# Kernel tuning notes

Hardware: AMD Instinct MI355X
Metric: run time of the kernel (lower is better)

Reference implementation:

```python
import jax, jax.numpy as jnp
import numpy as np

N_COMPANY = 16384
N_SECTOR = 64
PER_SECTOR = N_COMPANY // N_SECTOR  # 256, companies grouped contiguously by sector
WIN = 32
D_IN = 16
H_GRU = 64
H_INTRA = 64
H_INTER = 64
D_OUT = 4
E_INNER = 524288  # avg degree 32 within sectors


def setup_inputs() -> dict:
    key = jax.random.key(0)
    ks = jax.random.split(key, 20)
    s = 0.05

    daily_data_batch = jax.random.normal(ks[0], (WIN, N_COMPANY, D_IN), jnp.float32)

    rng = np.random.default_rng(0)
    dst = rng.integers(0, N_COMPANY, E_INNER)
    src = (dst // PER_SECTOR) * PER_SECTOR + rng.integers(0, PER_SECTOR, E_INNER)  # same-sector neighbors
    inner_edge = jnp.asarray(np.stack([src, dst]), jnp.int32)

    a, b = np.meshgrid(np.arange(N_SECTOR), np.arange(N_SECTOR), indexing="ij")
    oe = np.stack([a.ravel(), b.ravel()])
    oe = oe[:, oe[0] != oe[1]]  # fully-connected sector graph w/o self loops (GAT adds them)
    outer_edge = jnp.asarray(oe, jnp.int32)

    sector_ids = jnp.asarray(np.arange(N_COMPANY) // PER_SECTOR, jnp.int32)

    inp = {
        "daily_data_batch": daily_data_batch,
        "inner_edge": inner_edge,
        "outer_edge": outer_edge,
        "sector_ids": sector_ids,
        # BatchNorm1d(input_dim*window_size)
        "bn_gamma": jnp.ones((D_IN * WIN,), jnp.float32),
        "bn_beta": jnp.zeros((D_IN * WIN,), jnp.float32),
        # Graph GRU (per-node learnable initial hidden state)
        "gru_Wih": s * jax.random.normal(ks[1], (D_IN, 3 * H_GRU), jnp.float32),
        "gru_Whh": s * jax.random.normal(ks[2], (H_GRU, 3 * H_GRU), jnp.float32),
        "gru_bih": jnp.zeros((3 * H_GRU,), jnp.float32),
        "gru_bhh": jnp.zeros((3 * H_GRU,), jnp.float32),
        "gru_h0": s * jax.random.normal(ks[3], (N_COMPANY, H_GRU), jnp.float32),
        # intra-sector GATConv
        "gat1_W": s * jax.random.normal(ks[4], (H_GRU, H_INTRA), jnp.float32),
        "gat1_asrc": s * jax.random.normal(ks[5], (H_INTRA,), jnp.float32),
        "gat1_adst": s * jax.random.normal(ks[6], (H_INTRA,), jnp.float32),
        "gat1_b": jnp.zeros((H_INTRA,), jnp.float32),
        # inter-sector GATConv
        "gat2_W": s * jax.random.normal(ks[7], (H_INTRA, H_INTER), jnp.float32),
        "gat2_asrc": s * jax.random.normal(ks[8], (H_INTER,), jnp.float32),
        "gat2_adst": s * jax.random.normal(ks[9], (H_INTER,), jnp.float32),
        "gat2_b": jnp.zeros((H_INTER,), jnp.float32),
        # fusion / logit heads
        "fusion_W": s * jax.random.normal(ks[10], (H_GRU + H_INTRA + H_INTER, H_GRU), jnp.float32),
        "fusion_b": jnp.zeros((H_GRU,), jnp.float32),
        "logit_W": s * jax.random.normal(ks[11], (H_GRU, D_OUT), jnp.float32),
        "logit_b": jnp.zeros((D_OUT,), jnp.float32),
    }
    return inp


def _gat(x, edge, W, a_src, a_dst, b):
    """PyG-style single-head GATConv with default add_self_loops=True."""
    N = x.shape[0]
    h = x @ W  # [N, F]
    loops = jnp.arange(N, dtype=edge.dtype)
    src = jnp.concatenate([edge[0], loops])
    dst = jnp.concatenate([edge[1], loops])
    e = jax.nn.leaky_relu(h[src] @ a_src + h[dst] @ a_dst, 0.2)  # [E]
    # segment softmax over incoming edges per dst node
    m = jax.ops.segment_max(e, dst, num_segments=N)
    ex = jnp.exp(e - m[dst])
    denom = jax.ops.segment_sum(ex, dst, num_segments=N)
    alpha = ex / (denom[dst] + 1e-16)
    out = jax.ops.segment_sum(h[src] * alpha[:, None], dst, num_segments=N)
    return out + b


def _forward(daily_data_batch, inner_edge, outer_edge, sector_ids,
             bn_gamma, bn_beta,
             gru_Wih, gru_Whh, gru_bih, gru_bhh, gru_h0,
             gat1_W, gat1_asrc, gat1_adst, gat1_b,
             gat2_W, gat2_asrc, gat2_adst, gat2_b,
             fusion_W, fusion_b, logit_W, logit_b):
    W, N, D = daily_data_batch.shape
    # BatchNorm1d over companies (train-mode batch stats, eps=1e-5)
    xb = jnp.transpose(daily_data_batch, (1, 0, 2)).reshape(N, W * D)
    mu = xb.mean(axis=0)
    var = xb.var(axis=0)
    xb = (xb - mu) * jax.lax.rsqrt(var + 1e-5) * bn_gamma + bn_beta
    x = jnp.transpose(xb.reshape(N, W, D), (1, 0, 2))  # [W, N, D]

    # GRU over the window, per-node hidden state
    def step(h, xt):
        gi = xt @ gru_Wih + gru_bih
        gh = h @ gru_Whh + gru_bhh
        ir, iz, inn = jnp.split(gi, 3, axis=-1)
        hr, hz, hn = jnp.split(gh, 3, axis=-1)
        r = jax.nn.sigmoid(ir + hr)
        z = jax.nn.sigmoid(iz + hz)
        n = jnp.tanh(inn + r * hn)
        return (1.0 - z) * n + z * h, None

    seq_emb, _ = jax.lax.scan(step, gru_h0, x)  # [N, H_GRU]

    intra_emb = _gat(seq_emb, inner_edge, gat1_W, gat1_asrc, gat1_adst, gat1_b)  # [N, H_INTRA]

    # sector_separater + per-sector max pooling == segment_max
    sec_pool = jax.ops.segment_max(intra_emb, sector_ids, num_segments=N_SECTOR)  # [S, H_INTRA]
    sec_emb = _gat(sec_pool, outer_edge, gat2_W, gat2_asrc, gat2_adst, gat2_b)  # [S, H_INTER]
    sec_broad = sec_emb[sector_ids]  # repeat_interleave back to companies

    fusion_vec = jnp.concatenate([seq_emb, sec_broad, intra_emb], axis=-1)
    fusion_vec = jax.nn.relu(fusion_vec @ fusion_W + fusion_b)
    logits = jax.nn.softmax(fusion_vec @ logit_W + logit_b, axis=1)
    logits = jnp.cumsum(logits, axis=1)
    eps = 5e-08
    return jnp.clip(logits, eps, 1.0 - eps)


def reference(daily_data_batch, inner_edge, outer_edge, sector_ids,
              bn_gamma, bn_beta,
              gru_Wih, gru_Whh, gru_bih, gru_bhh, gru_h0,
              gat1_W, gat1_asrc, gat1_adst, gat1_b,
              gat2_W, gat2_asrc, gat2_adst, gat2_b,
              fusion_W, fusion_b, logit_W, logit_b):
    return _forward(daily_data_batch, inner_edge, outer_edge, sector_ids,
                    bn_gamma, bn_beta,
                    gru_Wih, gru_Whh, gru_bih, gru_bhh, gru_h0,
                    gat1_W, gat1_asrc, gat1_adst, gat1_b,
                    gat2_W, gat2_asrc, gat2_adst, gat2_b,
                    fusion_W, fusion_b, logit_W, logit_b)
```

## Files before the change

kernel.cpp:

```cpp
#include <hip/hip_runtime.h>

#define NC 16384
#define WIN 32
#define DI 16
#define EI 524288

typedef unsigned short u16;
typedef unsigned char u8;
typedef unsigned int u32;
typedef __attribute__((ext_vector_type(8))) short bfrag8;
typedef __attribute__((ext_vector_type(4))) float facc4;

__device__ __forceinline__ float bf2f(u16 u) { return __uint_as_float(((u32)u) << 16); }
__device__ __forceinline__ u16 f2bf(float f) {
    u32 u = __float_as_uint(f);
    u += 0x7FFFu + ((u >> 16) & 1u);
    return (u16)(u >> 16);
}
__device__ __forceinline__ float frcp(float x) { return __builtin_amdgcn_rcpf(x); }
__device__ __forceinline__ float lrelu(float x) { return x >= 0.0f ? x : 0.2f * x; }
__device__ __forceinline__ float loadf(const void* p, size_t i, bool f32) {
    return f32 ? ((const float*)p)[i] : bf2f(((const u16*)p)[i]);
}
__device__ __forceinline__ bool is_f32(const void* gamma) {
// ... 60 lines not shown
        ws[O_BHH + i] = loadf(bhh, i, f32);
    }
    for (int i = gt; i < 4096; i += GS) {
        ws[O_G1W + i] = loadf(g1w, i, f32);
        ws[O_G2W + i] = loadf(g2w, i, f32);
    }
    if (gt < 64) {
        ws[O_G1AS + gt] = loadf(g1as, gt, f32);
        ws[O_G1AD + gt] = loadf(g1ad, gt, f32);
        ws[O_G1B + gt] = loadf(g1b, gt, f32);
        ws[O_G2AS + gt] = loadf(g2as, gt, f32);
        ws[O_G2AD + gt] = loadf(g2ad, gt, f32);
        ws[O_G2B + gt] = loadf(g2b, gt, f32);
        ws[O_FB + gt] = loadf(fb, gt, f32);
    }
    if (gt < 256) ws[O_LW + gt] = loadf(lw, gt, f32);
    if (gt < 4) ws[O_LB + gt] = loadf(lb, gt, f32);
    for (int i = gt; i < 1024; i += GS) ws[O_BNACC + i] = 0.f;
    const uint4 z4 = {0u, 0u, 0u, 0u};
    for (int i = gt; i < 262144; i += GS) M16[i] = z4;
}

__global__ __launch_bounds__(256) void k_prep(const void* __restrict__ daily,
                                              const void* __restrict__ gamma,
                                              float* __restrict__ bnacc,
                                              const int* __restrict__ edges,
                                              u32* __restrict__ M32) {
    __shared__ float rS[256 * 17];
    __shared__ float rQ[256 * 17];
    int bid = blockIdx.x;
    int tid = threadIdx.x;
    if (bid >= 128) {
        int g = (bid - 128) * 256 + tid;
        int4 s4 = ((const int4*)edges)[g];
        int4 d4 = ((const int4*)(edges + EI))[g];
        int ss[4] = {s4.x, s4.y, s4.z, s4.w};
        int dd[4] = {d4.x, d4.y, d4.z, d4.w};
#pragma unroll
        for (int i = 0; i < 4; i++) {
            int sl = ss[i] & 255;
            atomicAdd(&M32[dd[i] * 64 + (sl >> 2)], 1u << ((sl & 3) * 8));
        }
        return;
    }
    int w = bid >> 2, ch = bid & 3;
    bool f32 = is_f32(gamma);
    float s[16], q[16];
#pragma unroll
    for (int i = 0; i < 16; i++) { s[i] = 0.f; q[i] = 0.f; }
    for (int it = 0; it < 16; it++) {
        int c = ch * 4096 + it * 256 + tid;
        size_t base = ((size_t)w * NC + c) * DI;
        float v[16];
        if (f32) {
            const float4* p = (const float4*)((const float*)daily + base);
            float4 a = p[0], b = p[1], cc = p[2], d = p[3];
            v[0] = a.x; v[1] = a.y; v[2] = a.z; v[3] = a.w;
            v[4] = b.x; v[5] = b.y; v[6] = b.z; v[7] = b.w;
            v[8] = cc.x; v[9] = cc.y; v[10] = cc.z; v[11] = cc.w;
            v[12] = d.x; v[13] = d.y; v[14] = d.z; v[15] = d.w;
        } else {
            const uint4* p = (const uint4*)((const u16*)daily + base);
            uint4 a = p[0], b = p[1];
            u32 us[8] = {a.x, a.y, a.z, a.w, b.x, b.y, b.z, b.w};
#pragma unroll
            for (int i = 0; i < 8; i++) {
                v[2 * i] = __uint_as_float(us[i] << 16);
                v[2 * i + 1] = __uint_as_float(us[i] & 0xFFFF0000u);
            }
        }
#pragma unroll
        for (int i = 0; i < 16; i++) { s[i] += v[i]; q[i] += v[i] * v[i]; }
    }
#pragma unroll
    for (int i = 0; i < 16; i++) { rS[tid * 17 + i] = s[i]; rQ[tid * 17 + i] = q[i]; }
    __syncthreads();
    int f = tid & 15, g = tid >> 4;
    float ss = 0.f, qq = 0.f;
    for (int t = g * 16; t < g * 16 + 16; t++) { ss += rS[t * 17 + f]; qq += rQ[t * 17 + f]; }
    atomicAdd(&bnacc[w * 16 + f], ss);
    atomicAdd(&bnacc[512 + w * 16 + f], qq);
}

__global__ __launch_bounds__(128, 2) void k_gru(const void* __restrict__ daily,
                                                const void* __restrict__ gamma,
                                                const void* __restrict__ beta,
                                                const void* __restrict__ h0_g,
                                                const float* __restrict__ ws,
                                                float* __restrict__ seq_out,
                                                u16* __restrict__ h1_out,
                                                float* __restrict__ asg,
                                                float* __restrict__ adg) {
    __shared__ __attribute__((aligned(16))) u16 sHd[2][16 * 72];
    __shared__ __attribute__((aligned(16))) u16 sXall[512 * 24];
    __shared__ float sSc[512], sSh[512];
    __shared__ float sRed[2][2][16];
    int tid = threadIdx.x;
    int w = tid >> 6, lane = tid & 63;
    int li = lane & 15, q = lane >> 4;
    int n0 = blockIdx.x * 16;
    bool f32 = is_f32(gamma);

    for (int f = tid; f < 512; f += 128) {
        float mu = ws[O_BNACC + f] * (1.0f / NC);
        float var = ws[O_BNACC + 512 + f] * (1.0f / NC) - mu * mu;
        float sc = loadf(gamma, f, f32) * rsqrtf(var + 1e-5f);
        sSc[f] = sc;
        sSh[f] = loadf(beta, f, f32) - mu * sc;
    }
    __syncthreads();
    for (int R = tid; R < 512; R += 128) {
        int t = R >> 4, m = R & 15;
        size_t base = ((size_t)t * NC + n0 + m) * DI;
        float xv[16];
        if (f32) {
            const float4* p = (const float4*)((const float*)daily + base);
            float4 a = p[0], b = p[1], c = p[2], d = p[3];
            xv[0] = a.x; xv[1] = a.y; xv[2] = a.z; xv[3] = a.w;
            xv[4] = b.x; xv[5] = b.y; xv[6] = b.z; xv[7] = b.w;
            xv[8] = c.x; xv[9] = c.y; xv[10] = c.z; xv[11] = c.w;
            xv[12] = d.x; xv[13] = d.y; xv[14] = d.z; xv[15] = d.w;
        } else {
            const uint4* p = (const uint4*)((const u16*)daily + base);
            uint4 a = p[0], b = p[1];
            u32 us[8] = {a.x, a.y, a.z, a.w, b.x, b.y, b.z, b.w};
#pragma unroll
            for (int i = 0; i < 8; i++) {
                xv[2 * i] = __uint_as_float(us[i] << 16);
                xv[2 * i + 1] = __uint_as_float(us[i] & 0xFFFF0000u);
            }
        }
        u16 px[16];
#pragma unroll
        for (int i = 0; i < 16; i++) px[i] = f2bf(xv[i] * sSc[t * 16 + i] + sSh[t * 16 + i]);
        *(uint4*)&sXall[R * 24] = *(const uint4*)&px[0];
        *(uint4*)&sXall[R * 24 + 8] = *(const uint4*)&px[8];
    }

    bfrag8 bh[3][2][2], bx[3][2];
#pragma unroll
    for (int g = 0; g < 3; g++) {
        float sc = (g < 2) ? -1.0f : -2.0f;
#pragma unroll
        for (int jt = 0; jt < 2; jt++) {
            int col = w * 32 + jt * 16 + li;
#pragma unroll
            for (int kc = 0; kc < 2; kc++)
#pragma unroll
                for (int j = 0; j < 8; j++) {
                    int k = kc * 32 + q * 8 + j;
                    bh[g][kc][jt][j] = (short)f2bf(sc * ws[O_WHH + k * 192 + g * 64 + col]);
                }
#pragma unroll
            for (int j = 0; j < 8; j++) {
                int k = q * 8 + j;
                bx[g][jt][j] = (k < 16) ? (short)f2bf(sc * ws[O_WIH + k * 192 + g * 64 + col]) : (short)0;
            }
        }
    }
    facc4 cR[2], cZ[2], cNX[2], cNH[2];
#pragma unroll
    for (int jt = 0; jt < 2; jt++) {
        int col = w * 32 + jt * 16 + li;
        float bR = -1.0f * (ws[O_BIH + col] + ws[O_BHH + col]);
        float bZ = -1.0f * (ws[O_BIH + 64 + col] + ws[O_BHH + 64 + col]);
        float bNX = -2.0f * ws[O_BIH + 128 + col];
        float bNH = -2.0f * ws[O_BHH + 128 + col];
        cR[jt] = (facc4){bR, bR, bR, bR};
        cZ[jt] = (facc4){bZ, bZ, bZ, bZ};
        cNX[jt] = (facc4){bNX, bNX, bNX, bNX};
        cNH[jt] = (facc4){bNH, bNH, bNH, bNH};
    }

    float hC[2][4];
#pragma unroll
    for (int jt = 0; jt < 2; jt++)
#pragma unroll
        for (int r = 0; r < 4; r++)
            hC[jt][r] = loadf(h0_g, (size_t)(n0 + q * 4 + r) * 64 + w * 32 + jt * 16 + li, f32);
    {
        int hr = tid >> 3, hc = (tid & 7) * 8;
        u16 hrow[8];
#pragma unroll
        for (int i = 0; i < 8; i++)
            hrow[i] = f2bf(loadf(h0_g, (size_t)(n0 + hr) * 64 + hc + i, f32));
        *(uint4*)&sHd[0][hr * 72 + hc] = *(const uint4*)&hrow[0];
    }
    __syncthreads();

    for (int t = 0; t < WIN; t++) {
        int p = t & 1;
        bfrag8 ah0 = *(const bfrag8*)&sHd[p][li * 72 + q * 8];
        bfrag8 ah1 = *(const bfrag8*)&sHd[p][li * 72 + 32 + q * 8];
        bfrag8 ax = {0, 0, 0, 0, 0, 0, 0, 0};
        if (q < 2) ax = *(const bfrag8*)&sXall[(t * 16 + li) * 24 + q * 8];
        facc4 aR[2], aZ[2], aNH[2], aNX[2];
#pragma unroll
        for (int jt = 0; jt < 2; jt++) {
            aR[jt] = __builtin_amdgcn_mfma_f32_16x16x32_bf16(ah0, bh[0][0][jt], cR[jt], 0, 0, 0);
            aZ[jt] = __builtin_amdgcn_mfma_f32_16x16x32_bf16(ah0, bh[1][0][jt], cZ[jt], 0, 0, 0);
            aNH[jt] = __builtin_amdgcn_mfma_f32_16x16x32_bf16(ah0, bh[2][0][jt], cNH[jt], 0, 0, 0);
            aNX[jt] = __builtin_amdgcn_mfma_f32_16x16x32_bf16(ax, bx[2][jt], cNX[jt], 0, 0, 0);
        }
#pragma unroll
        for (int jt = 0; jt < 2; jt++) {
            aR[jt] = __builtin_amdgcn_mfma_f32_16x16x32_bf16(ah1, bh[0][1][jt], aR[jt], 0, 0, 0);
            aZ[jt] = __builtin_amdgcn_mfma_f32_16x16x32_bf16(ah1, bh[1][1][jt], aZ[jt], 0, 0, 0);
            aNH[jt] = __builtin_amdgcn_mfma_f32_16x16x32_bf16(ah1, bh[2][1][jt], aNH[jt], 0, 0, 0);
        }
#pragma unroll
        for (int jt = 0; jt < 2; jt++) {
            aR[jt] = __builtin_amdgcn_mfma_f32_16x16x32_bf16(ax, bx[0][jt], aR[jt], 0, 0, 0);
            aZ[jt] = __builtin_amdgcn_mfma_f32_16x16x32_bf16(ax, bx[1][jt], aZ[jt], 0, 0, 0);
        }
#pragma unroll
        for (int jt = 0; jt < 2; jt++)
#pragma unroll
            for (int r = 0; r < 4; r++) {
                float gr = frcp(1.0f + __expf(aR[jt][r]));
                float gz = frcp(1.0f + __expf(aZ[jt][r]));
                float narg = aNX[jt][r] + gr * aNH[jt][r];
                float gn = 2.0f * frcp(1.0f + __expf(narg)) - 1.0f;
                hC[jt][r] = gn + gz * (hC[jt][r] - gn);
            }
#pragma unroll
        for (int jt = 0; jt < 2; jt++)
#pragma unroll
            for (int r = 0; r < 4; r++)
                sHd[p ^ 1][(q * 4 + r) * 72 + w * 32 + jt * 16 + li] = f2bf(hC[jt][r]);
        __syncthreads();
    }

#pragma unroll
    for (int jt = 0; jt < 2; jt++)
#pragma unroll
        for (int r = 0; r < 4; r++)
            seq_out[(size_t)(n0 + q * 4 + r) * 64 + w * 32 + jt * 16 + li] = hC[jt][r];

    const facc4 zf = {0.f, 0.f, 0.f, 0.f};
    bfrag8 a0 = *(const bfrag8*)&sHd[0][li * 72 + q * 8];
    bfrag8 a1 = *(const bfrag8*)&sHd[0][li * 72 + 32 + q * 8];
    float pAs[4] = {0.f, 0.f, 0.f, 0.f}, pAd[4] = {0.f, 0.f, 0.f, 0.f};
#pragma unroll
    for (int jt = 0; jt < 2; jt++) {
        int col = w * 32 + jt * 16 + li;
        bfrag8 bg0, bg1f;
#pragma unroll
        for (int j = 0; j < 8; j++) {
            bg0[j] = (short)f2bf(ws[O_G1W + (q * 8 + j) * 64 + col]);
            bg1f[j] = (short)f2bf(ws[O_G1W + (32 + q * 8 + j) * 64 + col]);
        }
        facc4 acc = __builtin_amdgcn_mfma_f32_16x16x32_bf16(a0, bg0, zf, 0, 0, 0);
        acc = __builtin_amdgcn_mfma_f32_16x16x32_bf16(a1, bg1f, acc, 0, 0, 0);
        float a1s_j = ws[O_G1AS + col], a1d_j = ws[O_G1AD + col];
#pragma unroll
        for (int r = 0; r < 4; r++) {
            h1_out[(size_t)(n0 + q * 4 + r) * 64 + col] = f2bf(acc[r]);
            pAs[r] += acc[r] * a1s_j;
            pAd[r] += acc[r] * a1d_j;
        }
    }
#pragma unroll
    for (int o = 1; o < 16; o <<= 1) {
#pragma unroll
        for (int r = 0; r < 4; r++) {
            pAs[r] += __shfl_xor(pAs[r], o);
            pAd[r] += __shfl_xor(pAd[r], o);
        }
    }
    if (li == 0) {
#pragma unroll
        for (int r = 0; r < 4; r++) {
            sRed[0][w][q * 4 + r] = pAs[r];
            sRed[1][w][q * 4 + r] = pAd[r];
        }
    }
    __syncthreads();
    if (tid < 16) {
        asg[n0 + tid] = sRed[0][0][tid] + sRed[0][1][tid];
        adg[n0 + tid] = sRed[1][0][tid] + sRed[1][1][tid];
    }
}

__global__ __launch_bounds__(256) void k_gat1agg(const u16* __restrict__ h1g,
                                                 const float* __restrict__ ws,
                                                 const u8* __restrict__ M8,
                                                 const float* __restrict__ asg,
                                                 const float* __restrict__ adg,
                                                 u16* __restrict__ intra,
                                                 float* __restrict__ spool4) {
    __shared__ __attribute__((aligned(16))) u16 hT[64 * 264];
    __shared__ float sAs[256], sAd[64], sB[64], sRS[64];
    __shared__ float wmax[4];
    int tid = threadIdx.x;
    int sector = blockIdx.x >> 2;
    int dstbase = sector * 256 + (blockIdx.x & 3) * 64;
    int sbase = sector * 256;
    {
        const u16* row = h1g + (size_t)(sbase + tid) * 64;
#pragma unroll
        for (int c = 0; c < 16; c++) {
            uint2 v = ((const uint2*)row)[c];
            hT[(c * 4 + 0) * 264 + tid] = (u16)(v.x & 0xffff);
            hT[(c * 4 + 1) * 264 + tid] = (u16)(v.x >> 16);
            hT[(c * 4 + 2) * 264 + tid] = (u16)(v.y & 0xffff);
            hT[(c * 4 + 3) * 264 + tid] = (u16)(v.y >> 16);
        }
    }
    sAs[tid] = asg[sbase + tid];
    if (tid < 64) { sAd[tid] = adg[dstbase + tid]; sB[tid] = ws[O_G1B + tid]; }
    __syncthreads();
    int lane = tid & 63, w = tid >> 6;
    int li = lane & 15, q = lane >> 4;
    {
        float a = sAs[tid];
#pragma unroll
        for (int o = 1; o < 64; o <<= 1) a = fmaxf(a, __shfl_xor(a, o));
        if (lane == 0) wmax[w] = a;
    }
    __syncthreads();
    float maxA = fmaxf(fmaxf(wmax[0], wmax[1]), fmaxf(wmax[2], wmax[3]));

    facc4 acc[4];
    float rs[4];
#pragma unroll
    for (int mt = 0; mt < 4; mt++) {
        acc[mt] = (facc4){0.f, 0.f, 0.f, 0.f};
        rs[mt] = 0.f;
    }
#pragma unroll
    for (int mt = 0; mt < 4; mt++) {
        int row = mt * 16 + li;
        float adr = sAd[row];
        float mrow = lrelu(maxA + adr);
        const u8* mrowp = M8 + (size_t)(dstbase + row) * 256;
#pragma unroll
        for (int kc = 0; kc < 8; kc++) {
            uint2 mv = *(const uint2*)(mrowp + kc * 32 + q * 8);
            bfrag8 af;
            float lsum = 0.f;
            u32 words[2] = {mv.x, mv.y};
#pragma unroll
            for (int j = 0; j < 8; j++) {
                u32 mb = (words[j >> 2] >> ((j & 3) * 8)) & 255u;
                float e = lrelu(sAs[kc * 32 + q * 8 + j] + adr);
                float v = (float)mb * __expf(e - mrow);
                u16 b = f2bf(v);
                af[j] = (short)b;
                lsum += bf2f(b);
            }
            bfrag8 bf = *(const bfrag8*)&hT[(w * 16 + li) * 264 + kc * 32 + q * 8];
            acc[mt] = __builtin_amdgcn_mfma_f32_16x16x32_bf16(af, bf, acc[mt], 0, 0, 0);
            rs[mt] += lsum;
        }
    }
#pragma unroll
    for (int mt = 0; mt < 4; mt++) {
        rs[mt] += __shfl_xor(rs[mt], 16);
        rs[mt] += __shfl_xor(rs[mt], 32);
    }
    if (w == 0 && q == 0) {
#pragma unroll
        for (int mt = 0; mt < 4; mt++) sRS[mt * 16 + li] = rs[mt];
    }
    __syncthreads();
    float vmax = -1e30f;
    int colL = w * 16 + li;
#pragma unroll
    for (int mt = 0; mt < 4; mt++) {
#pragma unroll
        for (int r = 0; r < 4; r++) {
            int row = mt * 16 + q * 4 + r;
            int d = dstbase + row;
            int selfI = (blockIdx.x & 3) * 64 + row;
            float adr = sAd[row];
            float es = lrelu(sAs[selfI] + adr);
            float mrow = lrelu(maxA + adr);
            float exS = __expf(es - mrow);
            float denom = sRS[row] + exS;
            float inv = frcp(denom + 1e-16f);
            float selfh = bf2f(hT[colL * 264 + selfI]);
            float val = (acc[mt][r] + exS * selfh) * inv + sB[colL];
            intra[(size_t)d * 64 + colL] = f2bf(val);
            vmax = fmaxf(vmax, val);
        }
    }
    vmax = fmaxf(vmax, __shfl_xor(vmax, 16));
    vmax = fmaxf(vmax, __shfl_xor(vmax, 32));
    if (q == 0) spool4[(size_t)blockIdx.x * 64 + colL] = vmax;
}

__global__ __launch_bounds__(256) void k_fusion(const float* __restrict__ seq,
                                                const float* __restrict__ spool4,
                                                const u16* __restrict__ intra,
                                                const float* __restrict__ ws,
                                                const void* __restrict__ gamma,
                                                void* __restrict__ out) {
    __shared__ __attribute__((aligned(16))) union {
        struct { float sPt[4096]; float sW2[4096]; float sH2[4096]; } p0;
        struct { u16 sV[12288]; u16 sWF[12288]; } p1;
    } U;
    __shared__ float sSemb[64], sAs2[64], sAd2[64];
    __shared__ float sFB[64], sLW[256], sLB[4];
    __shared__ float red[64 * 4 * 4];
    int tid = threadIdx.x, n0 = blockIdx.x * 64;
    int sid = blockIdx.x >> 2;
    bool f32 = is_f32(gamma);

    for (int i = tid; i < 4096; i += 256) {
        int n = i >> 6, k = i & 63;
        float m = fmaxf(fmaxf(spool4[(n * 4 + 0) * 64 + k], spool4[(n * 4 + 1) * 64 + k]),
                        fmaxf(spool4[(n * 4 + 2) * 64 + k], spool4[(n * 4 + 3) * 64 + k]));
        U.p0.sPt[k * 64 + n] = m;
        U.p0.sW2[i] = ws[O_G2W + i];
    }
    __syncthreads();
    {
        int n = tid >> 2, jg = tid & 3, j0 = jg * 16;
        float acc[16];
#pragma unroll
        for (int i = 0; i < 16; i++) acc[i] = 0.f;
        for (int k = 0; k < 64; k++) {
            float a = U.p0.sPt[k * 64 + n];
#pragma unroll
            for (int i = 0; i < 16; i += 4) {
                float4 w4 = *(const float4*)&U.p0.sW2[k * 64 + j0 + i];
                acc[i] += a * w4.x; acc[i + 1] += a * w4.y; acc[i + 2] += a * w4.z; acc[i + 3] += a * w4.w;
            }
        }
#pragma unroll
        for (int i = 0; i < 16; i++) U.p0.sH2[n * 64 + j0 + i] = acc[i];
        float ps = 0.f, pd = 0.f;
#pragma unroll
        for (int i = 0; i < 16; i++) { ps += acc[i] * ws[O_G2AS + j0 + i]; pd += acc[i] * ws[O_G2AD + j0 + i]; }
        red[(n * 4 + jg) * 2] = ps;
        red[(n * 4 + jg) * 2 + 1] = pd;
    }
    __syncthreads();
    if (tid < 64) {
        float s = 0.f, dd = 0.f;
        for (int g = 0; g < 4; g++) { s += red[(tid * 4 + g) * 2]; dd += red[(tid * 4 + g) * 2 + 1]; }
        sAs2[tid] = s; sAd2[tid] = dd;
    }
    __syncthreads();
    if (tid < 64) {
        float e = lrelu(sAs2[tid] + sAd2[sid]);
        float m = e;
        for (int o = 32; o; o >>= 1) m = fmaxf(m, __shfl_xor(m, o));
        float ex = __expf(e - m);
        float den = ex;
        for (int o = 32; o; o >>= 1) den += __shfl_xor(den, o);
        float inv = frcp(den + 1e-16f);
        float o_ = 0.f;
        for (int l = 0; l < 64; l++) {
            float a = __shfl(ex, l);
            o_ += a * U.p0.sH2[l * 64 + tid];
        }
        sSemb[tid] = o_ * inv + ws[O_G2B + tid];
    }
    __syncthreads();

    {
        const uint4* src = (const uint4*)(ws + O_FW16);
        uint4* dst = (uint4*)U.p1.sWF;
        for (int i = tid; i < 1536; i += 256) dst[i] = src[i];
    }
    if (tid < 64) sFB[tid] = ws[O_FB + tid];
    sLW[tid] = ws[O_LW + tid];
    if (tid < 4) sLB[tid] = ws[O_LB + tid];
    {
        int c = tid >> 2, p = tid & 3;
        {
            const float* rp = seq + (size_t)(n0 + c) * 64 + p * 16;
            int k0 = p * 16;
#pragma unroll
            for (int i = 0; i < 16; i += 4) {
                float4 v = *(const float4*)&rp[i];
                U.p1.sV[(k0 + i) * 64 + c] = f2bf(v.x);
                U.p1.sV[(k0 + i + 1) * 64 + c] = f2bf(v.y);
                U.p1.sV[(k0 + i + 2) * 64 + c] = f2bf(v.z);
                U.p1.sV[(k0 + i + 3) * 64 + c] = f2bf(v.w);
            }
        }
        {
            int k0 = 64 + p * 16;
#pragma unroll
            for (int i = 0; i < 16; i++)
                U.p1.sV[(k0 + i) * 64 + c] = f2bf(sSemb[p * 16 + i]);
        }
        {
            const u16* rp = intra + (size_t)(n0 + c) * 64 + p * 16;
            int k0 = 128 + p * 16;
            uint4 u0 = *(const uint4*)rp;
            uint4 u1 = *(const uint4*)(rp + 8);
            u32 arr[8] = {u0.x, u0.y, u0.z, u0.w, u1.x, u1.y, u1.z, u1.w};
#pragma unroll
            for (int ii = 0; ii < 8; ii++) {
                U.p1.sV[(k0 + 2 * ii) * 64 + c] = (u16)(arr[ii] & 0xffff);
                U.p1.sV[(k0 + 2 * ii + 1) * 64 + c] = (u16)(arr[ii] >> 16);
            }
        }
    }
    __syncthreads();
    int c = tid >> 2, jg = tid & 3, j0 = jg * 16;
    float acc[16];
#pragma unroll
    for (int i = 0; i < 16; i++) acc[i] = 0.f;
    for (int k = 0; k < 192; k++) {
        float v = bf2f(U.p1.sV[k * 64 + c]);
        const u16* wr = &U.p1.sWF[k * 64 + j0];
        ushort4 w0 = *(const ushort4*)wr;
        ushort4 w1 = *(const ushort4*)(wr + 4);
        ushort4 w2 = *(const ushort4*)(wr + 8);
        ushort4 w3 = *(const ushort4*)(wr + 12);
        acc[0] += v * bf2f(w0.x); acc[1] += v * bf2f(w0.y); acc[2] += v * bf2f(w0.z); acc[3] += v * bf2f(w0.w);
        acc[4] += v * bf2f(w1.x); acc[5] += v * bf2f(w1.y); acc[6] += v * bf2f(w1.z); acc[7] += v * bf2f(w1.w);
        acc[8] += v * bf2f(w2.x); acc[9] += v * bf2f(w2.y); acc[10] += v * bf2f(w2.z); acc[11] += v * bf2f(w2.w);
        acc[12] += v * bf2f(w3.x); acc[13] += v * bf2f(w3.y); acc[14] += v * bf2f(w3.z); acc[15] += v * bf2f(w3.w);
    }
    float p[4] = {0.f, 0.f, 0.f, 0.f};
#pragma unroll
    for (int i = 0; i < 16; i++) {
        float r = fmaxf(acc[i] + sFB[j0 + i], 0.f);
#pragma unroll
        for (int o = 0; o < 4; o++) p[o] += r * sLW[(j0 + i) * 4 + o];
    }
#pragma unroll
    for (int o = 0; o < 4; o++) red[(c * 4 + jg) * 4 + o] = p[o];
    __syncthreads();
    if (tid < 64) {
        float l[4];
#pragma unroll
        for (int o = 0; o < 4; o++) {
            float s = 0.f;
            for (int g = 0; g < 4; g++) s += red[(tid * 4 + g) * 4 + o];
            l[o] = s + sLB[o];
        }
        float m = fmaxf(fmaxf(l[0], l[1]), fmaxf(l[2], l[3]));
        float e0 = __expf(l[0] - m), e1 = __expf(l[1] - m), e2 = __expf(l[2] - m), e3 = __expf(l[3] - m);
        float is = frcp(e0 + e1 + e2 + e3);
        float c0 = e0 * is;
        float c1 = c0 + e1 * is;
        float c2 = c1 + e2 * is;
        float c3 = c2 + e3 * is;
        const float lo = 5e-8f, hi = 1.0f - 5e-8f;
        c0 = fminf(fmaxf(c0, lo), hi);
        c1 = fminf(fmaxf(c1, lo), hi);
        c2 = fminf(fmaxf(c2, lo), hi);
        c3 = fminf(fmaxf(c3, lo), hi);
        size_t ob = (size_t)(n0 + tid) * 4;
        if (f32) {
            *(float4*)&((float*)out)[ob] = make_float4(c0, c1, c2, c3);
        } else {
            *(ushort4*)&((u16*)out)[ob] = make_ushort4(f2bf(c0), f2bf(c1), f2bf(c2), f2bf(c3));
        }
    }
}

extern "C" void kernel_launch(void* const* d_in, const int* in_sizes, int n_in,
                              void* d_out, int out_size, void* d_ws, size_t ws_size,
                              hipStream_t stream) {
    const void* daily = d_in[0];
    const int* inner = (const int*)d_in[1];
    const void* gamma = d_in[4];
    const void* beta = d_in[5];
    const void* wih = d_in[6];
    const void* whh = d_in[7];
    const void* bih = d_in[8];
    const void* bhh = d_in[9];
    const void* h0 = d_in[10];
    const void* g1w = d_in[11];
    const void* g1as = d_in[12];
    const void* g1ad = d_in[13];
    const void* g1b = d_in[14];
    const void* g2w = d_in[15];
    const void* g2as = d_in[16];
    const void* g2ad = d_in[17];
    const void* g2b = d_in[18];
    const void* fw = d_in[19];
    const void* fb = d_in[20];
    const void* lw = d_in[21];
    const void* lb = d_in[22];

    float* ws = (float*)d_ws;
    u16* h1g = (u16*)(ws + O_H1);
    u16* intra = (u16*)(ws + O_INTRA);
    u8* M8 = (u8*)(ws + O_M);

    k_convert<<<64, 256, 0, stream>>>(gamma, wih, whh, bih, bhh, g1w, g1as, g1ad, g1b,
                                      g2w, g2as, g2ad, g2b, fw, fb, lw, lb, ws, (uint4*)M8);
    k_prep<<<640, 256, 0, stream>>>(daily, gamma, ws + O_BNACC, inner, (u32*)M8);
    k_gru<<<1024, 128, 0, stream>>>(daily, gamma, beta, h0, ws, ws + O_SEQ, h1g, ws + O_AS, ws + O_AD);
    k_gat1agg<<<256, 256, 0, stream>>>(h1g, ws, M8, ws + O_AS, ws + O_AD, intra, ws + O_SPOOL);
    k_fusion<<<256, 256, 0, stream>>>(ws + O_SEQ, ws + O_SPOOL, intra, ws, gamma, d_out);
}
```

Baseline: 245.0 us.

## Widen GRU to four waves, stage GAT probabilities in LDS, MFMA fusion matmul

The GRU kernel moves from 2 to 4 waves per 16-node block, each wave owning 16 hidden columns. The block-wide upfront staging of normalized inputs in shared memory is replaced by a per-step register prefetch that applies BN on the fly. The GAT aggregation now computes attention probabilities cooperatively into an LDS tile in two halves before the MFMA loop, instead of each wave recomputing them per fragment. The fusion kernel's scalar 192x64 FMA loop becomes bf16 MFMA with a row-major LDS layout, and the logit projection is moved to a per-row loop. These changes aim to raise parallelism in the serial GRU recurrence and cut redundant exp/ALU work, at the cost of extra barriers and more LDS traffic.

Measured after the change: 226.7 us. 7.5% less time.

```diff
diff --git a/kernel.cpp b/kernel.cpp
--- a/kernel.cpp
+++ b/kernel.cpp
@@ -166,7 +166,7 @@
     atomicAdd(&bnacc[512 + w * 16 + f], qq);
 }
 
-__global__ __launch_bounds__(128, 2) void k_gru(const void* __restrict__ daily,
+__global__ __launch_bounds__(256, 4) void k_gru(const void* __restrict__ daily,
                                                 const void* __restrict__ gamma,
                                                 const void* __restrict__ beta,
                                                 const void* __restrict__ h0_g,
@@ -176,93 +176,50 @@
                                                 float* __restrict__ asg,
                                                 float* __restrict__ adg) {
     __shared__ __attribute__((aligned(16))) u16 sHd[2][16 * 72];
-    __shared__ __attribute__((aligned(16))) u16 sXall[512 * 24];
     __shared__ float sSc[512], sSh[512];
-    __shared__ float sRed[2][2][16];
+    __shared__ float sRed[2][4][16];
     int tid = threadIdx.x;
     int w = tid >> 6, lane = tid & 63;
     int li = lane & 15, q = lane >> 4;
+    int col = w * 16 + li;
     int n0 = blockIdx.x * 16;
     bool f32 = is_f32(gamma);
 
-    for (int f = tid; f < 512; f += 128) {
+    for (int f = tid; f < 512; f += 256) {
         float mu = ws[O_BNACC + f] * (1.0f / NC);
         float var = ws[O_BNACC + 512 + f] * (1.0f / NC) - mu * mu;
         float sc = loadf(gamma, f, f32) * rsqrtf(var + 1e-5f);
         sSc[f] = sc;
         sSh[f] = loadf(beta, f, f32) - mu * sc;
     }
-    __syncthreads();
-    for (int R = tid; R < 512; R += 128) {
-        int t = R >> 4, m = R & 15;
-        size_t base = ((size_t)t * NC + n0 + m) * DI;
-        float xv[16];
-        if (f32) {
-            const float4* p = (const float4*)((const float*)daily + base);
-            float4 a = p[0], b = p[1], c = p[2], d = p[3];
-            xv[0] = a.x; xv[1] = a.y; xv[2] = a.z; xv[3] = a.w;
-            xv[4] = b.x; xv[5] = b.y; xv[6] = b.z; xv[7] = b.w;
-            xv[8] = c.x; xv[9] = c.y; xv[10] = c.z; xv[11] = c.w;
-            xv[12] = d.x; xv[13] = d.y; xv[14] = d.z; xv[15] = d.w;
-        } else {
-            const uint4* p = (const uint4*)((const u16*)daily + base);
-            uint4 a = p[0], b = p[1];
-            u32 us[8] = {a.x, a.y, a.z, a.w, b.x, b.y, b.z, b.w};
-#pragma unroll
-            for (int i = 0; i < 8; i++) {
-                xv[2 * i] = __uint_as_float(us[i] << 16);
-                xv[2 * i + 1] = __uint_as_float(us[i] & 0xFFFF0000u);
-            }
-        }
-        u16 px[16];
-#pragma unroll
-        for (int i = 0; i < 16; i++) px[i] = f2bf(xv[i] * sSc[t * 16 + i] + sSh[t * 16 + i]);
-        *(uint4*)&sXall[R * 24] = *(const uint4*)&px[0];
-        *(uint4*)&sXall[R * 24 + 8] = *(const uint4*)&px[8];
-    }
-
-    bfrag8 bh[3][2][2], bx[3][2];
+
+    bfrag8 bh[3][2], bx[3];
 #pragma unroll
     for (int g = 0; g < 3; g++) {
         float sc = (g < 2) ? -1.0f : -2.0f;
 #pragma unroll
-        for (int jt = 0; jt < 2; jt++) {
-            int col = w * 32 + jt * 16 + li;
-#pragma unroll
-            for (int kc = 0; kc < 2; kc++)
-#pragma unroll
-                for (int j = 0; j < 8; j++) {
-                    int k = kc * 32 + q * 8 + j;
-                    bh[g][kc][jt][j] = (short)f2bf(sc * ws[O_WHH + k * 192 + g * 64 + col]);
-                }
+        for (int kc = 0; kc < 2; kc++)
 #pragma unroll
             for (int j = 0; j < 8; j++) {
-                int k = q * 8 + j;
-                bx[g][jt][j] = (k < 16) ? (short)f2bf(sc * ws[O_WIH + k * 192 + g * 64 + col]) : (short)0;
+                int k = kc * 32 + q * 8 + j;
+                bh[g][kc][j] = (short)f2bf(sc * ws[O_WHH + k * 192 + g * 64 + col]);
             }
-        }
-    }
-    facc4 cR[2], cZ[2], cNX[2], cNH[2];
-#pragma unroll
-    for (int jt = 0; jt < 2; jt++) {
-        int col = w * 32 + jt * 16 + li;
-        float bR = -1.0f * (ws[O_BIH + col] + ws[O_BHH + col]);
-        float bZ = -1.0f * (ws[O_BIH + 64 + col] + ws[O_BHH + 64 + col]);
-        float bNX = -2.0f * ws[O_BIH + 128 + col];
-        float bNH = -2.0f * ws[O_BHH + 128 + col];
-        cR[jt] = (facc4){bR, bR, bR, bR};
-        cZ[jt] = (facc4){bZ, bZ, bZ, bZ};
-        cNX[jt] = (facc4){bNX, bNX, bNX, bNX};
-        cNH[jt] = (facc4){bNH, bNH, bNH, bNH};
-    }
-
-    float hC[2][4];
-#pragma unroll
-    for (int jt = 0; jt < 2; jt++)
-#pragma unroll
-        for (int r = 0; r < 4; r++)
-            hC[jt][r] = loadf(h0_g, (size_t)(n0 + q * 4 + r) * 64 + w * 32 + jt * 16 + li, f32);
-    {
+#pragma unroll
+        for (int j = 0; j < 8; j++) {
+            int k = q * 8 + j;
+            bx[g][j] = (k < 16) ? (short)f2bf(sc * ws[O_WIH + k * 192 + g * 64 + col]) : (short)0;
+        }
+    }
+    float bR = -1.0f * (ws[O_BIH + col] + ws[O_BHH + col]);
+    float bZ = -1.0f * (ws[O_BIH + 64 + col] + ws[O_BHH + 64 + col]);
+    float bNX = -2.0f * ws[O_BIH + 128 + col];
+    float bNH = -2.0f * ws[O_BHH + 128 + col];
+
+    float hC[4];
+#pragma unroll
+    for (int r = 0; r < 4; r++)
+        hC[r] = loadf(h0_g, (size_t)(n0 + q * 4 + r) * 64 + col, f32);
+    if (tid < 128) {
         int hr = tid >> 3, hc = (tid & 7) * 8;
         u16 hrow[8];
 #pragma unroll
@@ -272,77 +229,93 @@
     }
     __syncthreads();
 
+    bool xl = (q < 2);
+    float xr[8];
+    if (xl) {
+        size_t base = ((size_t)(n0 + li)) * DI + q * 8;
+        if (f32) {
+            float4 a = *(const float4*)((const float*)daily + base);
+            float4 b = *(const float4*)((const float*)daily + base + 4);
+            xr[0] = a.x; xr[1] = a.y; xr[2] = a.z; xr[3] = a.w;
+            xr[4] = b.x; xr[5] = b.y; xr[6] = b.z; xr[7] = b.w;
+        } else {
+            ushort4 a = *(const ushort4*)((const u16*)daily + base);
+            ushort4 b = *(const ushort4*)((const u16*)daily + base + 4);
+            xr[0] = bf2f(a.x); xr[1] = bf2f(a.y); xr[2] = bf2f(a.z); xr[3] = bf2f(a.w);
+            xr[4] = bf2f(b.x); xr[5] = bf2f(b.y); xr[6] = bf2f(b.z); xr[7] = bf2f(b.w);
+        }
+    }
+
     for (int t = 0; t < WIN; t++) {
         int p = t & 1;
+        bfrag8 ax = (bfrag8){0, 0, 0, 0, 0, 0, 0, 0};
+        if (xl) {
+            int sb = t * 16 + q * 8;
+#pragma unroll
+            for (int j = 0; j < 8; j++)
+                ax[j] = (short)f2bf(xr[j] * sSc[sb + j] + sSh[sb + j]);
+        }
         bfrag8 ah0 = *(const bfrag8*)&sHd[p][li * 72 + q * 8];
         bfrag8 ah1 = *(const bfrag8*)&sHd[p][li * 72 + 32 + q * 8];
-        bfrag8 ax = {0, 0, 0, 0, 0, 0, 0, 0};
-        if (q < 2) ax = *(const bfrag8*)&sXall[(t * 16 + li) * 24 + q * 8];
-        facc4 aR[2], aZ[2], aNH[2], aNX[2];
-#pragma unroll
-        for (int jt = 0; jt < 2; jt++) {
-            aR[jt] = __builtin_amdgcn_mfma_f32_16x16x32_bf16(ah0, bh[0][0][jt], cR[jt], 0, 0, 0);
-            aZ[jt] = __builtin_amdgcn_mfma_f32_16x16x32_bf16(ah0, bh[1][0][jt], cZ[jt], 0, 0, 0);
-            aNH[jt] = __builtin_amdgcn_mfma_f32_16x16x32_bf16(ah0, bh[2][0][jt], cNH[jt], 0, 0, 0);
-            aNX[jt] = __builtin_amdgcn_mfma_f32_16x16x32_bf16(ax, bx[2][jt], cNX[jt], 0, 0, 0);
-        }
-#pragma unroll
-        for (int jt = 0; jt < 2; jt++) {
-            aR[jt] = __builtin_amdgcn_mfma_f32_16x16x32_bf16(ah1, bh[0][1][jt], aR[jt], 0, 0, 0);
-            aZ[jt] = __builtin_amdgcn_mfma_f32_16x16x32_bf16(ah1, bh[1][1][jt], aZ[jt], 0, 0, 0);
-            aNH[jt] = __builtin_amdgcn_mfma_f32_16x16x32_bf16(ah1, bh[2][1][jt], aNH[jt], 0, 0, 0);
-        }
-#pragma unroll
-        for (int jt = 0; jt < 2; jt++) {
-            aR[jt] = __builtin_amdgcn_mfma_f32_16x16x32_bf16(ax, bx[0][jt], aR[jt], 0, 0, 0);
-            aZ[jt] = __builtin_amdgcn_mfma_f32_16x16x32_bf16(ax, bx[1][jt], aZ[jt], 0, 0, 0);
-        }
-#pragma unroll
-        for (int jt = 0; jt < 2; jt++)
-#pragma unroll
-            for (int r = 0; r < 4; r++) {
-                float gr = frcp(1.0f + __expf(aR[jt][r]));
-                float gz = frcp(1.0f + __expf(aZ[jt][r]));
-                float narg = aNX[jt][r] + gr * aNH[jt][r];
-                float gn = 2.0f * frcp(1.0f + __expf(narg)) - 1.0f;
-                hC[jt][r] = gn + gz * (hC[jt][r] - gn);
+        if (xl && t < WIN - 1) {
+            size_t base = ((size_t)(t + 1) * NC + n0 + li) * DI + q * 8;
+            if (f32) {
+                float4 a = *(const float4*)((const float*)daily + base);
+                float4 b = *(const float4*)((const float*)daily + base + 4);
+                xr[0] = a.x; xr[1] = a.y; xr[2] = a.z; xr[3] = a.w;
+                xr[4] = b.x; xr[5] = b.y; xr[6] = b.z; xr[7] = b.w;
+            } else {
+                ushort4 a = *(const ushort4*)((const u16*)daily + base);
+                ushort4 b = *(const ushort4*)((const u16*)daily + base + 4);
+                xr[0] = bf2f(a.x); xr[1] = bf2f(a.y); xr[2] = bf2f(a.z); xr[3] = bf2f(a.w);
+                xr[4] = bf2f(b.x); xr[5] = bf2f(b.y); xr[6] = bf2f(b.z); xr[7] = bf2f(b.w);
             }
-#pragma unroll
-        for (int jt = 0; jt < 2; jt++)
-#pragma unroll
-            for (int r = 0; r < 4; r++)
-                sHd[p ^ 1][(q * 4 + r) * 72 + w * 32 + jt * 16 + li] = f2bf(hC[jt][r]);
+        }
+        facc4 aR = __builtin_amdgcn_mfma_f32_16x16x32_bf16(ah0, bh[0][0], (facc4){bR, bR, bR, bR}, 0, 0, 0);
+        facc4 aZ = __builtin_amdgcn_mfma_f32_16x16x32_bf16(ah0, bh[1][0], (facc4){bZ, bZ, bZ, bZ}, 0, 0, 0);
+        facc4 aNH = __builtin_amdgcn_mfma_f32_16x16x32_bf16(ah0, bh[2][0], (facc4){bNH, bNH, bNH, bNH}, 0, 0, 0);
+        facc4 aNX = __builtin_amdgcn_mfma_f32_16x16x32_bf16(ax, bx[2], (facc4){bNX, bNX, bNX, bNX}, 0, 0, 0);
+        aR = __builtin_amdgcn_mfma_f32_16x16x32_bf16(ah1, bh[0][1], aR, 0, 0, 0);
+        aZ = __builtin_amdgcn_mfma_f32_16x16x32_bf16(ah1, bh[1][1], aZ, 0, 0, 0);
+        aNH = __builtin_amdgcn_mfma_f32_16x16x32_bf16(ah1, bh[2][1], aNH, 0, 0, 0);
+        aR = __builtin_amdgcn_mfma_f32_16x16x32_bf16(ax, bx[0], aR, 0, 0, 0);
+        aZ = __builtin_amdgcn_mfma_f32_16x16x32_bf16(ax, bx[1], aZ, 0, 0, 0);
+#pragma unroll
+        for (int r = 0; r < 4; r++) {
+            float gr = frcp(1.0f + __expf(aR[r]));
+            float gz = frcp(1.0f + __expf(aZ[r]));
+            float narg = aNX[r] + gr * aNH[r];
+            float gn = 2.0f * frcp(1.0f + __expf(narg)) - 1.0f;
+            hC[r] = gn + gz * (hC[r] - gn);
+        }
+#pragma unroll
+        for (int r = 0; r < 4; r++)
+            sHd[p ^ 1][(q * 4 + r) * 72 + col] = f2bf(hC[r]);
         __syncthreads();
     }
 
 #pragma unroll
-    for (int jt = 0; jt < 2; jt++)
-#pragma unroll
-        for (int r = 0; r < 4; r++)
-            seq_out[(size_t)(n0 + q * 4 + r) * 64 + w * 32 + jt * 16 + li] = hC[jt][r];
+    for (int r = 0; r < 4; r++)
+        seq_out[(size_t)(n0 + q * 4 + r) * 64 + col] = hC[r];
 
     const facc4 zf = {0.f, 0.f, 0.f, 0.f};
     bfrag8 a0 = *(const bfrag8*)&sHd[0][li * 72 + q * 8];
     bfrag8 a1 = *(const bfrag8*)&sHd[0][li * 72 + 32 + q * 8];
-    float pAs[4] = {0.f, 0.f, 0.f, 0.f}, pAd[4] = {0.f, 0.f, 0.f, 0.f};
-#pragma unroll
-    for (int jt = 0; jt < 2; jt++) {
-        int col = w * 32 + jt * 16 + li;
-        bfrag8 bg0, bg1f;
-#pragma unroll
-        for (int j = 0; j < 8; j++) {
-            bg0[j] = (short)f2bf(ws[O_G1W + (q * 8 + j) * 64 + col]);
-            bg1f[j] = (short)f2bf(ws[O_G1W + (32 + q * 8 + j) * 64 + col]);
-        }
-        facc4 acc = __builtin_amdgcn_mfma_f32_16x16x32_bf16(a0, bg0, zf, 0, 0, 0);
-        acc = __builtin_amdgcn_mfma_f32_16x16x32_bf16(a1, bg1f, acc, 0, 0, 0);
-        float a1s_j = ws[O_G1AS + col], a1d_j = ws[O_G1AD + col];
-#pragma unroll
-        for (int r = 0; r < 4; r++) {
-            h1_out[(size_t)(n0 + q * 4 + r) * 64 + col] = f2bf(acc[r]);
-            pAs[r] += acc[r] * a1s_j;
-            pAd[r] += acc[r] * a1d_j;
-        }
+    bfrag8 bg0, bg1;
+#pragma unroll
+    for (int j = 0; j < 8; j++) {
+        bg0[j] = (short)f2bf(ws[O_G1W + (q * 8 + j) * 64 + col]);
+        bg1[j] = (short)f2bf(ws[O_G1W + (32 + q * 8 + j) * 64 + col]);
+    }
+    facc4 acc = __builtin_amdgcn_mfma_f32_16x16x32_bf16(a0, bg0, zf, 0, 0, 0);
+    acc = __builtin_amdgcn_mfma_f32_16x16x32_bf16(a1, bg1, acc, 0, 0, 0);
+    float a1s_j = ws[O_G1AS + col], a1d_j = ws[O_G1AD + col];
+    float pAs[4], pAd[4];
+#pragma unroll
+    for (int r = 0; r < 4; r++) {
+        h1_out[(size_t)(n0 + q * 4 + r) * 64 + col] = f2bf(acc[r]);
+        pAs[r] = acc[r] * a1s_j;
+        pAd[r] = acc[r] * a1d_j;
     }
 #pragma unroll
     for (int o = 1; o < 16; o <<= 1) {
@@ -361,8 +334,8 @@
     }
     __syncthreads();
     if (tid < 16) {
-        asg[n0 + tid] = sRed[0][0][tid] + sRed[0][1][tid];
-        adg[n0 + tid] = sRed[1][0][tid] + sRed[1][1][tid];
+        asg[n0 + tid] = sRed[0][0][tid] + sRed[0][1][tid] + sRed[0][2][tid] + sRed[0][3][tid];
+        adg[n0 + tid] = sRed[1][0][tid] + sRed[1][1][tid] + sRed[1][2][tid] + sRed[1][3][tid];
     }
 }
 
@@ -374,7 +347,9 @@
                                                  u16* __restrict__ intra,
                                                  float* __restrict__ spool4) {
     __shared__ __attribute__((aligned(16))) u16 hT[64 * 264];
+    __shared__ __attribute__((aligned(16))) u16 sP[64 * 136];
     __shared__ float sAs[256], sAd[64], sB[64], sRS[64];
+    __shared__ float sRSp[4][64];
     __shared__ float wmax[4];
     int tid = threadIdx.x;
     int sector = blockIdx.x >> 2;
@@ -405,49 +380,52 @@
     __syncthreads();
     float maxA = fmaxf(fmaxf(wmax[0], wmax[1]), fmaxf(wmax[2], wmax[3]));
 
+    int prow = tid >> 2, pcg = tid & 3;
+    float adr_p = sAd[prow];
+    float mrow_p = lrelu(maxA + adr_p);
+    float lsum = 0.f;
+
     facc4 acc[4];
-    float rs[4];
-#pragma unroll
-    for (int mt = 0; mt < 4; mt++) {
-        acc[mt] = (facc4){0.f, 0.f, 0.f, 0.f};
-        rs[mt] = 0.f;
-    }
-#pragma unroll
-    for (int mt = 0; mt < 4; mt++) {
-        int row = mt * 16 + li;
-        float adr = sAd[row];
-        float mrow = lrelu(maxA + adr);
-        const u8* mrowp = M8 + (size_t)(dstbase + row) * 256;
-#pragma unroll
-        for (int kc = 0; kc < 8; kc++) {
-            uint2 mv = *(const uint2*)(mrowp + kc * 32 + q * 8);
-            bfrag8 af;
-            float lsum = 0.f;
-            u32 words[2] = {mv.x, mv.y};
-#pragma unroll
-            for (int j = 0; j < 8; j++) {
-                u32 mb = (words[j >> 2] >> ((j & 3) * 8)) & 255u;
-                float e = lrelu(sAs[kc * 32 + q * 8 + j] + adr);
-                float v = (float)mb * __expf(e - mrow);
-                u16 b = f2bf(v);
-                af[j] = (short)b;
-                lsum += bf2f(b);
+#pragma unroll
+    for (int mt = 0; mt < 4; mt++) acc[mt] = (facc4){0.f, 0.f, 0.f, 0.f};
+
+#pragma unroll
+    for (int half = 0; half < 2; half++) {
+        const u8* mp = M8 + (size_t)(dstbase + prow) * 256 + half * 128 + pcg * 32;
+        uint4 mva = *(const uint4*)mp;
+        uint4 mvb = *(const uint4*)(mp + 16);
+        u32 wsrc[8] = {mva.x, mva.y, mva.z, mva.w, mvb.x, mvb.y, mvb.z, mvb.w};
+#pragma unroll
+        for (int i2 = 0; i2 < 16; i2++) {
+            int i0 = 2 * i2;
+            u32 mb0 = (wsrc[i0 >> 2] >> ((i0 & 3) * 8)) & 255u;
+            u32 mb1 = (wsrc[i0 >> 2] >> (((i0 + 1) & 3) * 8)) & 255u;
+            int c = half * 128 + pcg * 32 + i0;
+            float e0 = lrelu(sAs[c] + adr_p);
+            float e1 = lrelu(sAs[c + 1] + adr_p);
+            float v0 = (float)mb0 * __expf(e0 - mrow_p);
+            float v1 = (float)mb1 * __expf(e1 - mrow_p);
+            u16 b0 = f2bf(v0), b1 = f2bf(v1);
+            *(u32*)&sP[prow * 136 + pcg * 32 + i0] = (u32)b0 | ((u32)b1 << 16);
+            lsum += bf2f(b0) + bf2f(b1);
+        }
+        __syncthreads();
+#pragma unroll
+        for (int kc = 0; kc < 4; kc++) {
+            bfrag8 bfh = *(const bfrag8*)&hT[(w * 16 + li) * 264 + half * 128 + kc * 32 + q * 8];
+#pragma unroll
+            for (int mt = 0; mt < 4; mt++) {
+                bfrag8 af = *(const bfrag8*)&sP[(mt * 16 + li) * 136 + kc * 32 + q * 8];
+                acc[mt] = __builtin_amdgcn_mfma_f32_16x16x32_bf16(af, bfh, acc[mt], 0, 0, 0);
             }
-            bfrag8 bf = *(const bfrag8*)&hT[(w * 16 + li) * 264 + kc * 32 + q * 8];
-            acc[mt] = __builtin_amdgcn_mfma_f32_16x16x32_bf16(af, bf, acc[mt], 0, 0, 0);
-            rs[mt] += lsum;
-        }
-    }
-#pragma unroll
-    for (int mt = 0; mt < 4; mt++) {
-        rs[mt] += __shfl_xor(rs[mt], 16);
-        rs[mt] += __shfl_xor(rs[mt], 32);
-    }
-    if (w == 0 && q == 0) {
-#pragma unroll
-        for (int mt = 0; mt < 4; mt++) sRS[mt * 16 + li] = rs[mt];
-    }
-    __syncthreads();
+        }
+        __syncthreads();
+    }
+    sRSp[pcg][prow] = lsum;
+    __syncthreads();
+    if (tid < 64) sRS[tid] = sRSp[0][tid] + sRSp[1][tid] + sRSp[2][tid] + sRSp[3][tid];
+    __syncthreads();
+
     float vmax = -1e30f;
     int colL = w * 16 + li;
 #pragma unroll
@@ -482,11 +460,11 @@
                                                 void* __restrict__ out) {
     __shared__ __attribute__((aligned(16))) union {
         struct { float sPt[4096]; float sW2[4096]; float sH2[4096]; } p0;
-        struct { u16 sV[12288]; u16 sWF[12288]; } p1;
+        struct { u16 sV[64 * 200]; float sFus[64 * 68]; } p1;
     } U;
     __shared__ float sSemb[64], sAs2[64], sAd2[64];
     __shared__ float sFB[64], sLW[256], sLB[4];
-    __shared__ float red[64 * 4 * 4];
+    __shared__ float red2[512];
     int tid = threadIdx.x, n0 = blockIdx.x * 64;
     int sid = blockIdx.x >> 2;
     bool f32 = is_f32(gamma);
@@ -501,29 +479,29 @@
     __syncthreads();
     {
         int n = tid >> 2, jg = tid & 3, j0 = jg * 16;
-        float acc[16];
-#pragma unroll
-        for (int i = 0; i < 16; i++) acc[i] = 0.f;
+        float acc0[16];
+#pragma unroll
+        for (int i = 0; i < 16; i++) acc0[i] = 0.f;
         for (int k = 0; k < 64; k++) {
             float a = U.p0.sPt[k * 64 + n];
 #pragma unroll
             for (int i = 0; i < 16; i += 4) {
                 float4 w4 = *(const float4*)&U.p0.sW2[k * 64 + j0 + i];
-                acc[i] += a * w4.x; acc[i + 1] += a * w4.y; acc[i + 2] += a * w4.z; acc[i + 3] += a * w4.w;
+                acc0[i] += a * w4.x; acc0[i + 1] += a * w4.y; acc0[i + 2] += a * w4.z; acc0[i + 3] += a * w4.w;
             }
         }
 #pragma unroll
-        for (int i = 0; i < 16; i++) U.p0.sH2[n * 64 + j0 + i] = acc[i];
+        for (int i = 0; i < 16; i++) U.p0.sH2[n * 64 + j0 + i] = acc0[i];
         float ps = 0.f, pd = 0.f;
 #pragma unroll
-        for (int i = 0; i < 16; i++) { ps += acc[i] * ws[O_G2AS + j0 + i]; pd += acc[i] * ws[O_G2AD + j0 + i]; }
-        red[(n * 4 + jg) * 2] = ps;
-        red[(n * 4 + jg) * 2 + 1] = pd;
+        for (int i = 0; i < 16; i++) { ps += acc0[i] * ws[O_G2AS + j0 + i]; pd += acc0[i] * ws[O_G2AD + j0 + i]; }
+        red2[(n * 4 + jg) * 2] = ps;
+        red2[(n * 4 + jg) * 2 + 1] = pd;
     }
     __syncthreads();
     if (tid < 64) {
         float s = 0.f, dd = 0.f;
-        for (int g = 0; g < 4; g++) { s += red[(tid * 4 + g) * 2]; dd += red[(tid * 4 + g) * 2 + 1]; }
+        for (int g = 0; g < 4; g++) { s += red2[(tid * 4 + g) * 2]; dd += red2[(tid * 4 + g) * 2 + 1]; }
         sAs2[tid] = s; sAd2[tid] = dd;
     }
     __syncthreads();
@@ -542,83 +520,71 @@
         }
         sSemb[tid] = o_ * inv + ws[O_G2B + tid];
     }
-    __syncthreads();
-
-    {
-        const uint4* src = (const uint4*)(ws + O_FW16);
-        uint4* dst = (uint4*)U.p1.sWF;
-        for (int i = tid; i < 1536; i += 256) dst[i] = src[i];
-    }
     if (tid < 64) sFB[tid] = ws[O_FB + tid];
     sLW[tid] = ws[O_LW + tid];
     if (tid < 4) sLB[tid] = ws[O_LB + tid];
+    __syncthreads();
+
     {
         int c = tid >> 2, p = tid & 3;
-        {
-            const float* rp = seq + (size_t)(n0 + c) * 64 + p * 16;
-            int k0 = p * 16;
-#pragma unroll
-            for (int i = 0; i < 16; i += 4) {
-                float4 v = *(const float4*)&rp[i];
-                U.p1.sV[(k0 + i) * 64 + c] = f2bf(v.x);
-                U.p1.sV[(k0 + i + 1) * 64 + c] = f2bf(v.y);
-                U.p1.sV[(k0 + i + 2) * 64 + c] = f2bf(v.z);
-                U.p1.sV[(k0 + i + 3) * 64 + c] = f2bf(v.w);
-            }
-        }
-        {
-            int k0 = 64 + p * 16;
-#pragma unroll
-            for (int i = 0; i < 16; i++)
-                U.p1.sV[(k0 + i) * 64 + c] = f2bf(sSemb[p * 16 + i]);
-        }
-        {
-            const u16* rp = intra + (size_t)(n0 + c) * 64 + p * 16;
-            int k0 = 128 + p * 16;
-            uint4 u0 = *(const uint4*)rp;
-            uint4 u1 = *(const uint4*)(rp + 8);
-            u32 arr[8] = {u0.x, u0.y, u0.z, u0.w, u1.x, u1.y, u1.z, u1.w};
-#pragma unroll
-            for (int ii = 0; ii < 8; ii++) {
-                U.p1.sV[(k0 + 2 * ii) * 64 + c] = (u16)(arr[ii] & 0xffff);
-                U.p1.sV[(k0 + 2 * ii + 1) * 64 + c] = (u16)(arr[ii] >> 16);
-            }
-        }
-    }
-    __syncthreads();
-    int c = tid >> 2, jg = tid & 3, j0 = jg * 16;
-    float acc[16];
-#pragma unroll
-    for (int i = 0; i < 16; i++) acc[i] = 0.f;
-    for (int k = 0; k < 192; k++) {
-        float v = bf2f(U.p1.sV[k * 64 + c]);
-        const u16* wr = &U.p1.sWF[k * 64 + j0];
-        ushort4 w0 = *(const ushort4*)wr;
-        ushort4 w1 = *(const ushort4*)(wr + 4);
-        ushort4 w2 = *(const ushort4*)(wr + 8);
-        ushort4 w3 = *(const ushort4*)(wr + 12);
-        acc[0] += v * bf2f(w0.x); acc[1] += v * bf2f(w0.y); acc[2] += v * bf2f(w0.z); acc[3] += v * bf2f(w0.w);
-        acc[4] += v * bf2f(w1.x); acc[5] += v * bf2f(w1.y); acc[6] += v * bf2f(w1.z); acc[7] += v * bf2f(w1.w);
-        acc[8] += v * bf2f(w2.x); acc[9] += v * bf2f(w2.y); acc[10] += v * bf2f(w2.z); acc[11] += v * bf2f(w2.w);
-        acc[12] += v * bf2f(w3.x); acc[13] += v * bf2f(w3.y); acc[14] += v * bf2f(w3.z); acc[15] += v * bf2f(w3.w);
-    }
-    float p[4] = {0.f, 0.f, 0.f, 0.f};
-#pragma unroll
-    for (int i = 0; i < 16; i++) {
-        float r = fmaxf(acc[i] + sFB[j0 + i], 0.f);
-#pragma unroll
-        for (int o = 0; o < 4; o++) p[o] += r * sLW[(j0 + i) * 4 + o];
-    }
-#pragma unroll
-    for (int o = 0; o < 4; o++) red[(c * 4 + jg) * 4 + o] = p[o];
-    __syncthreads();
+        u16 px[16];
+        const float* rp = seq + (size_t)(n0 + c) * 64 + p * 16;
+#pragma unroll
+        for (int i = 0; i < 16; i += 4) {
+            float4 v = *(const float4*)&rp[i];
+            px[i] = f2bf(v.x); px[i + 1] = f2bf(v.y); px[i + 2] = f2bf(v.z); px[i + 3] = f2bf(v.w);
+        }
+        *(uint4*)&U.p1.sV[c * 200 + p * 16] = *(const uint4*)&px[0];
+        *(uint4*)&U.p1.sV[c * 200 + p * 16 + 8] = *(const uint4*)&px[8];
+#pragma unroll
+        for (int i = 0; i < 16; i++) px[i] = f2bf(sSemb[p * 16 + i]);
+        *(uint4*)&U.p1.sV[c * 200 + 64 + p * 16] = *(const uint4*)&px[0];
+        *(uint4*)&U.p1.sV[c * 200 + 64 + p * 16 + 8] = *(const uint4*)&px[8];
+        const u16* ip = intra + (size_t)(n0 + c) * 64 + p * 16;
+        *(uint4*)&U.p1.sV[c * 200 + 128 + p * 16] = *(const uint4*)ip;
+        *(uint4*)&U.p1.sV[c * 200 + 128 + p * 16 + 8] = *(const uint4*)(ip + 8);
+    }
+    int lane = tid & 63, w = tid >> 6;
+    int li = lane & 15, q = lane >> 4;
+    int colw = w * 16 + li;
+    const u16* fw16g = (const u16*)(ws + O_FW16);
+    bfrag8 bwf[6];
+#pragma unroll
+    for (int kc = 0; kc < 6; kc++)
+#pragma unroll
+        for (int j = 0; j < 8; j++)
+            bwf[kc][j] = (short)fw16g[(kc * 32 + q * 8 + j) * 64 + colw];
+    __syncthreads();
+
+    facc4 acc[4];
+#pragma unroll
+    for (int mt = 0; mt < 4; mt++) acc[mt] = (facc4){0.f, 0.f, 0.f, 0.f};
+#pragma unroll
+    for (int kc = 0; kc < 6; kc++) {
+#pragma unroll
+        for (int mt = 0; mt < 4; mt++) {
+            bfrag8 av = *(const bfrag8*)&U.p1.sV[(mt * 16 + li) * 200 + kc * 32 + q * 8];
+            acc[mt] = __builtin_amdgcn_mfma_f32_16x16x32_bf16(av, bwf[kc], acc[mt], 0, 0, 0);
+        }
+    }
+    float fb = sFB[colw];
+#pragma unroll
+    for (int mt = 0; mt < 4; mt++)
+#pragma unroll
+        for (int r = 0; r < 4; r++) {
+            float v = fmaxf(acc[mt][r] + fb, 0.f);
+            U.p1.sFus[(mt * 16 + q * 4 + r) * 68 + colw] = v;
+        }
+    __syncthreads();
+
     if (tid < 64) {
-        float l[4];
-#pragma unroll
-        for (int o = 0; o < 4; o++) {
-            float s = 0.f;
-            for (int g = 0; g < 4; g++) s += red[(tid * 4 + g) * 4 + o];
-            l[o] = s + sLB[o];
+        float l[4] = {sLB[0], sLB[1], sLB[2], sLB[3]};
+        for (int j = 0; j < 64; j++) {
+            float v = U.p1.sFus[tid * 68 + j];
+            l[0] += v * sLW[j * 4 + 0];
+            l[1] += v * sLW[j * 4 + 1];
+            l[2] += v * sLW[j * 4 + 2];
+            l[3] += v * sLW[j * 4 + 3];
         }
         float m = fmaxf(fmaxf(l[0], l[1]), fmaxf(l[2], l[3]));
         float e0 = __expf(l[0] - m), e1 = __expf(l[1] - m), e2 = __expf(l[2] - m), e3 = __expf(l[3] - m);
@@ -674,7 +640,7 @@
     k_convert<<<64, 256, 0, stream>>>(gamma, wih, whh, bih, bhh, g1w, g1as, g1ad, g1b,
                                       g2w, g2as, g2ad, g2b, fw, fb, lw, lb, ws, (uint4*)M8);
     k_prep<<<640, 256, 0, stream>>>(daily, gamma, ws + O_BNACC, inner, (u32*)M8);
-    k_gru<<<1024, 128, 0, stream>>>(daily, gamma, beta, h0, ws, ws + O_SEQ, h1g, ws + O_AS, ws + O_AD);
+    k_gru<<<1024, 256, 0, stream>>>(daily, gamma, beta, h0, ws, ws + O_SEQ, h1g, ws + O_AS, ws + O_AD);
     k_gat1agg<<<256, 256, 0, stream>>>(h1g, ws, M8, ws + O_AS, ws + O_AD, intra, ws + O_SPOOL);
     k_fusion<<<256, 256, 0, stream>>>(ws + O_SEQ, ws + O_SPOOL, intra, ws, gamma, d_out);
 }
```
